# Performance work log

Hardware: AMD Instinct MI355X
Metric: run time of the kernel (lower is better)

The kernel has to match this reference:

```python
import jax, jax.numpy as jnp
import numpy as np

TOP_K = 8            # num_experts_epr_tok
N_GROUP = 8
TOP_K_GROUP = 4
ROUTED_SCALING = 2.5
NORM_TOPK_PROB = True
T, H, E = 16384, 2048, 256


def setup_inputs() -> dict:
    key = jax.random.key(0)
    k1, k2 = jax.random.split(key)
    hidden_states = jax.random.normal(k1, (T, H), dtype=jnp.float32)
    weight = jax.random.normal(k2, (E, H), dtype=jnp.float32) * 0.02
    e_score_correction_bias = jnp.zeros((E,), dtype=jnp.float32)
    return {
        "hidden_states": hidden_states,
        "weight": weight,
        "e_score_correction_bias": e_score_correction_bias,
    }


def _route(h, w, b):
    t, e = h.shape[0], w.shape[0]
    per_group = e // N_GROUP
    # router logits in fp32, sigmoid gate (DeepSeek-V3 noaux_tc style)
    logits = jnp.einsum('th,eh->te', h.astype(jnp.float32), w.astype(jnp.float32))
    scores = jax.nn.sigmoid(logits)                       # [T, E]
    sfc = scores + b[None, :]                             # scores_for_choice
    # group score = sum of top-2 corrected scores within each group
    grouped = sfc.reshape(t, N_GROUP, per_group)
    top2, _ = jax.lax.top_k(grouped, 2)                   # [T, G, 2]
    group_scores = top2.sum(axis=-1)                      # [T, G]
    # select top groups, build expert mask
    _, group_idx = jax.lax.top_k(group_scores, TOP_K_GROUP)   # [T, Kg]
    group_mask = jax.nn.one_hot(group_idx, N_GROUP, dtype=jnp.bool_).any(axis=1)  # [T, G]
    score_mask = jnp.repeat(group_mask, per_group, axis=1)    # [T, E]
    masked = jnp.where(score_mask, sfc, 0.0)
    # top-k experts among allowed groups; weights gathered from UNcorrected scores
    _, top_k_indices = jax.lax.top_k(masked, TOP_K)           # [T, K]
    top_k_weights = jnp.take_along_axis(scores, top_k_indices, axis=1)
    if NORM_TOPK_PROB:
        top_k_weights = top_k_weights / (top_k_weights.sum(-1, keepdims=True) + 1e-20)
    top_k_weights = top_k_weights * ROUTED_SCALING
    return top_k_indices, top_k_weights


def reference(hidden_states, weight, e_score_correction_bias):
    return _route(hidden_states, weight, e_score_correction_bias)
```

## Files before the change

### kernel.cpp

```cpp
#include <hip/hip_runtime.h>
#include <math.h>

#define H_      2048
#define E_      256
#define T_TILE  32
#define KC      32
#define TOPK    8
#define KGROUP  4

typedef float f2 __attribute__((ext_vector_type(2)));

__device__ __forceinline__ void pk_fma(f2& a, f2 h, f2 w) {
    asm("v_pk_fma_f32 %0, %1, %2, %0" : "+v"(a) : "v"(h), "v"(w));
}

struct GemmSmem {
    float w[E_][KC];
    float h[T_TILE][KC];
};
union SMem {
    GemmSmem g;
    float logits[T_TILE][E_];
};

__global__ __launch_bounds__(256, 2)
void router_kernel(const float* __restrict__ hp,
                   const float* __restrict__ wp,
                   const float* __restrict__ bp,
                   float* __restrict__ out, int T)
{
#pragma clang fp contract(off)
    __shared__ SMem sm;
    const int tid  = threadIdx.x;
    const int t0   = blockIdx.x * T_TILE;
    const int lane = tid & 63;
    const int eq   = lane;
    const int wv   = tid >> 6;
    const int wvu  = __builtin_amdgcn_readfirstlane(wv);

    f2 acc[8][4][2];
#pragma unroll
    for (int i = 0; i < 8; ++i)
#pragma unroll
        for (int j = 0; j < 4; ++j) {
            acc[i][j][0] = (f2){0.f, 0.f};
            acc[i][j][1] = (f2){0.f, 0.f};
        }

    const float* wlds = &sm.g.w[eq << 2][0];
    const int    swx  = eq & 7;
    const float* hlds = &sm.g.h[wvu << 3][0];

    for (int ch = 0; ch < H_ / KC; ++ch) {
        const int k0 = ch * KC;

        {
            const float* src = hp + (size_t)(t0 + (wvu << 3) + (lane >> 3)) * H_
                             + k0 + ((lane & 7) << 2);
            __builtin_amdgcn_global_load_lds(
                (const __attribute__((address_space(1))) void*)src,
                (__attribute__((address_space(3))) void*)&sm.g.h[wvu << 3][0],
                16, 0, 0);
        }
#pragma unroll
        for (int r = 0; r < 8; ++r) {
            const int E0 = (r * 4 + wvu) * 8;
            const int e  = E0 + (lane >> 3);
            const int gs = (lane & 7) ^ ((e >> 2) & 7);
            const float* src = wp + (size_t)e * H_ + k0 + (gs << 2);
            __builtin_amdgcn_global_load_lds(
                (const __attribute__((address_space(1))) void*)src,
                (__attribute__((address_space(3))) void*)&sm.g.w[E0][0],
                16, 0, 0);
        }
        __syncthreads();

#pragma unroll
        for (int mb = 0; mb < 2; ++mb) {
#pragma unroll
            for (int jj = 3; jj >= 0; --jj) {
                const int S = (mb << 2) + jj;
                const float* wr = wlds + ((S ^ swx) << 2);
                float4 wreg[4];
                wreg[0] = *(const float4*)(wr);
                wreg[1] = *(const float4*)(wr + KC);
                wreg[2] = *(const float4*)(wr + 2 * KC);
                wreg[3] = *(const float4*)(wr + 3 * KC);
#pragma unroll
                for (int i = 0; i < 8; ++i) {
                    const float4 hv = *(const float4*)(hlds + i * KC + (S << 2));
                    const f2 hA = {hv.x, hv.y};
                    const f2 hB = {hv.z, hv.w};
#pragma unroll
                    for (int j = 0; j < 4; ++j) {
                        const f2 wA = {wreg[j].x, wreg[j].y};
                        const f2 wB = {wreg[j].z, wreg[j].w};
                        pk_fma(acc[i][j][0], hA, wA);
                        pk_fma(acc[i][j][1], hB, wB);
                    }
                }
            }
        }
        __syncthreads();
    }

#pragma unroll
    for (int i = 0; i < 8; ++i)
#pragma unroll
        for (int j = 0; j < 4; ++j)
            sm.logits[(wv << 3) + i][(eq << 2) + j] =
                ((acc[i][j][0].x + acc[i][j][0].y) +
                 (acc[i][j][1].x + acc[i][j][1].y));
    __syncthreads();

    float* out_idx = out;
    float* out_w   = out + (size_t)T * TOPK;

    const float b0 = bp[lane * 4 + 0];
    const float b1 = bp[lane * 4 + 1];
    const float b2 = bp[lane * 4 + 2];
    const float b3 = bp[lane * 4 + 3];

    for (int tt = 0; tt < 8; ++tt) {
        const int tl = (wv << 3) + tt;
        const int t  = t0 + tl;

        float4 lg = *(const float4*)(&sm.logits[tl][lane * 4]);
        const float E0 = (float)exp(-(double)lg.x);
        const float E1 = (float)exp(-(double)lg.y);
        const float E2 = (float)exp(-(double)lg.z);
        const float E3 = (float)exp(-(double)lg.w);
        const float s0 = __fdiv_rn(1.0f, __fadd_rn(1.0f, E0));
        const float s1 = __fdiv_rn(1.0f, __fadd_rn(1.0f, E1));
        const float s2 = __fdiv_rn(1.0f, __fadd_rn(1.0f, E2));
        const float s3 = __fdiv_rn(1.0f, __fadd_rn(1.0f, E3));
        const float f0 = s0 + b0, f1 = s1 + b1, f2 = s2 + b2, f3 = s3 + b3;

        float a = fmaxf(f0, f1), b = fminf(f0, f1);
        if (f2 > a) { b = a; a = f2; } else b = fmaxf(b, f2);
        if (f3 > a) { b = a; a = f3; } else b = fmaxf(b, f3);
#pragma unroll
        for (int m = 1; m <= 4; m <<= 1) {
            float oa = __shfl_xor(a, m);
            float ob = __shfl_xor(b, m);
            float na, nb;
            if (a >= oa) { na = a;  nb = fmaxf(oa, b); }
            else         { na = oa; nb = fmaxf(a, ob); }
            a = na; b = nb;
        }
        const float gsc = a + b;

        float g0 = __shfl(gsc,  0), g1 = __shfl(gsc,  8);
        float g2 = __shfl(gsc, 16), g3 = __shfl(gsc, 24);
        float g4 = __shfl(gsc, 32), g5 = __shfl(gsc, 40);
        float g6 = __shfl(gsc, 48), g7 = __shfl(gsc, 56);

        unsigned gmask = 0;
#pragma unroll
        for (int r = 0; r < KGROUP; ++r) {
            float best = g0; int bg = 0;
            if (g1 > best) { best = g1; bg = 1; }
            if (g2 > best) { best = g2; bg = 2; }
            if (g3 > best) { best = g3; bg = 3; }
            if (g4 > best) { best = g4; bg = 4; }
            if (g5 > best) { best = g5; bg = 5; }
            if (g6 > best) { best = g6; bg = 6; }
            if (g7 > best) { best = g7; bg = 7; }
            gmask |= (1u << bg);
            g0 = (bg == 0) ? -1.f : g0;  g1 = (bg == 1) ? -1.f : g1;
            g2 = (bg == 2) ? -1.f : g2;  g3 = (bg == 3) ? -1.f : g3;
            g4 = (bg == 4) ? -1.f : g4;  g5 = (bg == 5) ? -1.f : g5;
            g6 = (bg == 6) ? -1.f : g6;  g7 = (bg == 7) ? -1.f : g7;
        }

        const int  myg  = lane >> 3;
        const bool keep = (gmask >> myg) & 1u;
        float v0 = keep ? f0 : 0.f, v1 = keep ? f1 : 0.f;
        float v2 = keep ? f2 : 0.f, v3 = keep ? f3 : 0.f;

        int   isel[TOPK];
        float ssel[TOPK];
#pragma unroll
        for (int r = 0; r < TOPK; ++r) {
            float bv = v0; int bj = 0; float bs = s0;
            if (v1 > bv) { bv = v1; bj = 1; bs = s1; }
            if (v2 > bv) { bv = v2; bj = 2; bs = s2; }
            if (v3 > bv) { bv = v3; bj = 3; bs = s3; }
            float cv = bv; int ci = lane * 4 + bj; float cs = bs;
#pragma unroll
            for (int m = 1; m < 64; m <<= 1) {
                float ov = __shfl_xor(cv, m);
                int   oi = __shfl_xor(ci, m);
                float os = __shfl_xor(cs, m);
                if (ov > cv || (ov == cv && oi < ci)) { cv = ov; ci = oi; cs = os; }
            }
            isel[r] = ci; ssel[r] = cs;
            if ((ci >> 2) == lane) {
                const int sl = ci & 3;
                v0 = (sl == 0) ? -1.f : v0;
                v1 = (sl == 1) ? -1.f : v1;
                v2 = (sl == 2) ? -1.f : v2;
                v3 = (sl == 3) ? -1.f : v3;
            }
        }

        const float sum = __fadd_rn(
            __fadd_rn(__fadd_rn(ssel[0], ssel[1]), __fadd_rn(ssel[2], ssel[3])),
            __fadd_rn(__fadd_rn(ssel[4], ssel[5]), __fadd_rn(ssel[6], ssel[7])));
        const float denom = __fadd_rn(sum, 1e-20f);
        if (lane == 0) {
#pragma unroll
            for (int r = 0; r < TOPK; ++r) {
                out_idx[(size_t)t * TOPK + r] = (float)isel[r];
                out_w  [(size_t)t * TOPK + r] =
                    __fmul_rn(__fdiv_rn(ssel[r], denom), 2.5f);
            }
        }
    }
}

extern "C" void kernel_launch(void* const* d_in, const int* in_sizes, int n_in,
                              void* d_out, int out_size, void* d_ws, size_t ws_size,
                              hipStream_t stream) {
    const float* hs = (const float*)d_in[0];
    const float* w  = (const float*)d_in[1];
    const float* b  = (const float*)d_in[2];
    const int E = in_sizes[2];
    const int H = in_sizes[1] / E;
    const int T = in_sizes[0] / H;
    (void)n_in; (void)d_ws; (void)ws_size; (void)out_size; (void)E; (void)H;

    dim3 grid(T / T_TILE);
    router_kernel<<<grid, 256, 0, stream>>>(hs, w, b, (float*)d_out, T);
}
```

Measured before the change: 419.0 us.

## Load hidden-state tile to registers and broadcast via readlane into SGPR FMAs

Stops staging the hidden-state tile in LDS. Each lane now loads its float4 of the token row straight into registers, prefetching the next chunk one step ahead. The values are broadcast with v_readlane into scalar registers and fed as SGPR operands to v_pk_fma_f32. This removes LDS reads and LDS traffic for the activations, but adds four readlane instructions per token row per slice, and the readlane-to-VALU dependency can stall. Launch bounds also drop to one block per SM, which allows more registers at the cost of occupancy.

```diff
diff --git a/kernel.cpp b/kernel.cpp
--- a/kernel.cpp
+++ b/kernel.cpp
@@ -10,20 +10,17 @@
 
 typedef float f2 __attribute__((ext_vector_type(2)));
 
-__device__ __forceinline__ void pk_fma(f2& a, f2 h, f2 w) {
-    asm("v_pk_fma_f32 %0, %1, %2, %0" : "+v"(a) : "v"(h), "v"(w));
+__device__ __forceinline__ void pk_fma_s(f2& a, unsigned long long h, f2 w) {
+    asm("v_pk_fma_f32 %0, %1, %2, %0" : "+v"(a) : "s"(h), "v"(w));
 }
 
-struct GemmSmem {
-    float w[E_][KC];
-    float h[T_TILE][KC];
-};
+struct GemmSmem { float w[E_][KC]; };
 union SMem {
     GemmSmem g;
     float logits[T_TILE][E_];
 };
 
-__global__ __launch_bounds__(256, 2)
+__global__ __launch_bounds__(256, 1)
 void router_kernel(const float* __restrict__ hp,
                    const float* __restrict__ wp,
                    const float* __restrict__ bp,
@@ -49,19 +46,15 @@
 
     const float* wlds = &sm.g.w[eq << 2][0];
     const int    swx  = eq & 7;
-    const float* hlds = &sm.g.h[wvu << 3][0];
+
+    const float* hsrc0 = hp + (size_t)(t0 + (wvu << 3) + (lane >> 3)) * H_
+                       + ((lane & 7) << 2);
+
+    float4 hv = *(const float4*)(hsrc0);
 
     for (int ch = 0; ch < H_ / KC; ++ch) {
         const int k0 = ch * KC;
 
-        {
-            const float* src = hp + (size_t)(t0 + (wvu << 3) + (lane >> 3)) * H_
-                             + k0 + ((lane & 7) << 2);
-            __builtin_amdgcn_global_load_lds(
-                (const __attribute__((address_space(1))) void*)src,
-                (__attribute__((address_space(3))) void*)&sm.g.h[wvu << 3][0],
-                16, 0, 0);
-        }
 #pragma unroll
         for (int r = 0; r < 8; ++r) {
             const int E0 = (r * 4 + wvu) * 8;
@@ -75,6 +68,9 @@
         }
         __syncthreads();
 
+        const int chn = (ch < H_ / KC - 1) ? ch + 1 : ch;
+        float4 hv_next = *(const float4*)(hsrc0 + chn * KC);
+
 #pragma unroll
         for (int mb = 0; mb < 2; ++mb) {
 #pragma unroll
@@ -88,19 +84,30 @@
                 wreg[3] = *(const float4*)(wr + 3 * KC);
 #pragma unroll
                 for (int i = 0; i < 8; ++i) {
-                    const float4 hv = *(const float4*)(hlds + i * KC + (S << 2));
-                    const f2 hA = {hv.x, hv.y};
-                    const f2 hB = {hv.z, hv.w};
+                    const int sl = i * 8 + S;
+                    const unsigned hx = __builtin_amdgcn_readlane(
+                        __float_as_uint(hv.x), sl);
+                    const unsigned hy = __builtin_amdgcn_readlane(
+                        __float_as_uint(hv.y), sl);
+                    const unsigned hz = __builtin_amdgcn_readlane(
+                        __float_as_uint(hv.z), sl);
+                    const unsigned hw = __builtin_amdgcn_readlane(
+                        __float_as_uint(hv.w), sl);
+                    const unsigned long long hA =
+                        (unsigned long long)hx | ((unsigned long long)hy << 32);
+                    const unsigned long long hB =
+                        (unsigned long long)hz | ((unsigned long long)hw << 32);
 #pragma unroll
                     for (int j = 0; j < 4; ++j) {
                         const f2 wA = {wreg[j].x, wreg[j].y};
                         const f2 wB = {wreg[j].z, wreg[j].w};
-                        pk_fma(acc[i][j][0], hA, wA);
-                        pk_fma(acc[i][j][1], hB, wB);
+                        pk_fma_s(acc[i][j][0], hA, wA);
+                        pk_fma_s(acc[i][j][1], hB, wB);
                     }
                 }
             }
         }
+        hv = hv_next;
         __syncthreads();
     }
 
```

Measured after the change: 456.2 us. 1.09x slower.
